# Performance work log

Measured on AMD Instinct MI355X. Metric: run time of the kernel, lower is better.

## Reference

```python
import jax, jax.numpy as jnp
import numpy as np

N_HEAD = 16
ROPE_BASE = 10000.0
RMS_EPS = 1e-6

def rms_norm(x):
    # F.rms_norm(x, (x.size(-1),)) -- no learned weight
    return x * jax.lax.rsqrt(jnp.mean(x * x, axis=-1, keepdims=True) + RMS_EPS)

def rope(x):
    # x: [B, T, H, hd]; rotate halves (non-interleaved) like the torch Rotary
    T, hd = x.shape[1], x.shape[3]
    d = hd // 2
    inv_freq = 1.0 / (ROPE_BASE ** (jnp.arange(0, hd, 2, dtype=jnp.float32) / hd))  # [d]
    t = jnp.arange(T, dtype=jnp.float32)
    freqs = jnp.outer(t, inv_freq)                       # [T, d]
    cos = jnp.cos(freqs)[None, :, None, :]
    sin = jnp.sin(freqs)[None, :, None, :]
    x1, x2 = x[..., :d], x[..., d:]
    y1 = x1 * cos + x2 * sin
    y2 = -x1 * sin + x2 * cos
    return jnp.concatenate([y1, y2], axis=-1).astype(x.dtype)

def setup_inputs() -> dict:
    key = jax.random.key(0)
    ks = jax.random.split(key, 7)
    B, T, D, H = 2, 2048, 1024, N_HEAD
    hd = D // H
    s = 0.02
    return {
        "x": jax.random.normal(ks[0], (B, T, D), jnp.float32),
        "v1": jax.random.normal(ks[1], (B, T, H, hd), jnp.float32),
        "w_q": jax.random.normal(ks[2], (D, D), jnp.float32) * s,
        "w_k": jax.random.normal(ks[3], (D, D), jnp.float32) * s,
        "w_v": jax.random.normal(ks[4], (D, D), jnp.float32) * s,
        "w_proj": jax.random.normal(ks[5], (D, D), jnp.float32) * s,
        "lamb": jnp.float32(0.5),
    }

def reference(x, v1, w_q, w_k, w_v, w_proj, lamb):
    B, T, D = x.shape
    H = N_HEAD
    hd = D // H
    q = (x @ w_q.T).reshape(B, T, H, hd)
    k = (x @ w_k.T).reshape(B, T, H, hd)
    v = (x @ w_v.T).reshape(B, T, H, hd)
    v = (1.0 - lamb) * v + lamb * v1.reshape(B, T, H, hd)
    q, k = rms_norm(q), rms_norm(k)
    q, k = rope(q), rope(k)
    scale = 1.0 / jnp.sqrt(jnp.float32(hd))
    scores = jnp.einsum('bqhd,bkhd->bhqk', q, k) * scale  # [B,H,T,T]
    causal = jnp.tril(jnp.ones((T, T), dtype=bool))
    scores = jnp.where(causal[None, None], scores, jnp.float32(-1e30))
    attn = jax.nn.softmax(scores, axis=-1)
    y = jnp.einsum('bhqk,bkhd->bqhd', attn, v).reshape(B, T, D)
    y = y @ w_proj.T
    return (y, v1)
```

## Files before the change

kernel.cpp:

```cpp
#include <hip/hip_runtime.h>

typedef __bf16 bf16x8 __attribute__((ext_vector_type(8)));
typedef float f32x4 __attribute__((ext_vector_type(4)));
typedef float f32x16 __attribute__((ext_vector_type(16)));

__device__ __forceinline__ unsigned short f2bf(float f) {
    return __builtin_bit_cast(unsigned short, (__bf16)f);
}

__device__ __forceinline__ float bf2f(unsigned short u) {
    unsigned int x = ((unsigned int)u) << 16;
    return __builtin_bit_cast(float, x);
}

__device__ __forceinline__ unsigned int packbf2(float a, float b) {
    unsigned short lo = f2bf(a), hi = f2bf(b);
    return (unsigned int)lo | ((unsigned int)hi << 16);
}

__device__ __forceinline__ bf16x8 load_frag(const unsigned short* p) {
    int4 v = *reinterpret_cast<const int4*>(p);
    return __builtin_bit_cast(bf16x8, v);
}

__device__ __forceinline__ void gload_lds16(const unsigned short* g, unsigned short* l) {
    __builtin_amdgcn_global_load_lds((const __attribute__((address_space(1))) void*)g,
                                     (__attribute__((address_space(3))) void*)l, 16, 0, 0);
}

__global__ __launch_bounds__(256) void prep_bf16(const float* __restrict__ x,
                                                 const float* __restrict__ wq,
                                                 const float* __restrict__ wk,
                                                 const float* __restrict__ wv,
                                                 const float* __restrict__ wp,
                                                 unsigned short* __restrict__ xb,
                                                 unsigned short* __restrict__ wall,
                                                 float* __restrict__ cost,
                                                 float* __restrict__ sint) {
    int bid = blockIdx.x;
    if (bid < 8192) {
        int i = (bid * 256 + threadIdx.x) * 4;
        const float* src;
        unsigned short* dst;
        int soff, doff;
        if (i < (1 << 22)) {
            src = x; dst = xb; soff = i; doff = i;
        } else {
            int j = i - (1 << 22);
            int r = j >> 20;
            src = (r == 0) ? wq : ((r == 1) ? wk : ((r == 2) ? wv : wp));
            dst = wall; soff = j & 1048575; doff = j;
        }
        float4 v = *reinterpret_cast<const float4*>(&src[soff]);
        unsigned short tmp[4] = {f2bf(v.x), f2bf(v.y), f2bf(v.z), f2bf(v.w)};
        *reinterpret_cast<int2*>(&dst[doff]) = *reinterpret_cast<int2*>(tmp);
    } else {
        int i = (bid - 8192) * 256 + threadIdx.x;
        int t = i >> 5, d = i & 31;
        float inv = powf(10000.0f, -(float)d / 32.0f);
        float f = (float)t * inv;
        cost[i] = cosf(f);
        sint[i] = sinf(f);
    }
}

__global__ __launch_bounds__(256) void gemm_bf16(const unsigned short* __restrict__ A,
                                                 const unsigned short* __restrict__ B,
                                                 unsigned short* __restrict__ C,
                                                 int N, int K) {
    __shared__ __align__(16) unsigned short As[128 * 64];
    __shared__ __align__(16) unsigned short Bs[128 * 64];
    int tid = threadIdx.x;
    int lane = tid & 63;
    int w = tid >> 6;
    int wm = w >> 1, wn = w & 1;
    int m0 = blockIdx.x * 128;
    int n0 = blockIdx.y * 128;

    f32x4 acc[4][4] = {};

    int r8 = lane >> 3;
    int csrc = (lane & 7) ^ r8;

    for (int k0 = 0; k0 < K; k0 += 64) {
        __syncthreads();
#pragma unroll
        for (int c = 0; c < 4; ++c) {
            int row = 32 * w + 8 * c + r8;
            gload_lds16(&A[(size_t)(m0 + row) * K + k0 + csrc * 8], &As[(32 * w + 8 * c) * 64]);
            gload_lds16(&B[(size_t)(n0 + row) * K + k0 + csrc * 8], &Bs[(32 * w + 8 * c) * 64]);
        }
        __syncthreads();
#pragma unroll
        for (int kk = 0; kk < 2; ++kk) {
            int col16 = kk * 4 + (lane >> 4);
            bf16x8 af[4], bfr[4];
#pragma unroll
            for (int i = 0; i < 4; ++i) {
                int row = wm * 64 + i * 16 + (lane & 15);
                af[i] = load_frag(&As[row * 64 + (col16 ^ (row & 7)) * 8]);
            }
#pragma unroll
            for (int j = 0; j < 4; ++j) {
                int row = wn * 64 + j * 16 + (lane & 15);
                bfr[j] = load_frag(&Bs[row * 64 + (col16 ^ (row & 7)) * 8]);
            }
#pragma unroll
            for (int i = 0; i < 4; ++i)
#pragma unroll
                for (int j = 0; j < 4; ++j)
                    acc[i][j] = __builtin_amdgcn_mfma_f32_16x16x32_bf16(af[i], bfr[j], acc[i][j], 0, 0, 0);
        }
    }
    int r0 = (lane >> 4) * 4;
    int cc = lane & 15;
#pragma unroll
    for (int i = 0; i < 4; ++i)
#pragma unroll
        for (int j = 0; j < 4; ++j)
#pragma unroll
            for (int r = 0; r < 4; ++r) {
                size_t m = m0 + wm * 64 + i * 16 + r0 + r;
                size_t n = n0 + wn * 64 + j * 16 + cc;
                C[m * N + n] = f2bf(acc[i][j][r]);
            }
}

__global__ __launch_bounds__(256) void gemm_proj(const unsigned short* __restrict__ pO,
                                                 const float* __restrict__ lsum,
                                                 const unsigned short* __restrict__ B,
                                                 float* __restrict__ C) {
    __shared__ __align__(16) unsigned short As[128 * 64];
    __shared__ __align__(16) unsigned short Bs[128 * 64];
    int tid = threadIdx.x;
    int lane = tid & 63;
    int w = tid >> 6;
    int wm = w >> 1, wn = w & 1;
    int m0 = blockIdx.x * 128;
    int n0 = blockIdx.y * 128;

    f32x4 acc[4][4] = {};

    int r8 = lane >> 3;
    int c8 = lane & 7;
    int csrc = c8 ^ r8;

    for (int k0 = 0; k0 < 1024; k0 += 64) {
        int h = k0 >> 6;
        __syncthreads();
#pragma unroll
        for (int c = 0; c < 4; ++c) {
            int row = 32 * w + 8 * c + r8;
            int m = m0 + row;
            int bh = ((m >> 11) << 4) + h;
            int qi = m & 2047;
            int li = bh * 2048 + qi;
            size_t pi = (size_t)li * 64 + csrc * 8;
            int4 p0 = *reinterpret_cast<const int4*>(&pO[pi]);
            int4 p1 = *reinterpret_cast<const int4*>(&pO[4194304u + pi]);
            float linv = 1.0f / (lsum[li] + lsum[65536 + li]);
            const unsigned short* u0 = reinterpret_cast<const unsigned short*>(&p0);
            const unsigned short* u1 = reinterpret_cast<const unsigned short*>(&p1);
            unsigned short tmp[8];
#pragma unroll
            for (int j = 0; j < 8; ++j) tmp[j] = f2bf((bf2f(u0[j]) + bf2f(u1[j])) * linv);
            *reinterpret_cast<int4*>(&As[row * 64 + c8 * 8]) = *reinterpret_cast<int4*>(tmp);
            gload_lds16(&B[(size_t)(n0 + row) * 1024 + k0 + csrc * 8], &Bs[(32 * w + 8 * c) * 64]);
        }
        __syncthreads();
#pragma unroll
        for (int kk = 0; kk < 2; ++kk) {
            int col16 = kk * 4 + (lane >> 4);
            bf16x8 af[4], bfr[4];
#pragma unroll
            for (int i = 0; i < 4; ++i) {
                int row = wm * 64 + i * 16 + (lane & 15);
                af[i] = load_frag(&As[row * 64 + (col16 ^ (row & 7)) * 8]);
            }
#pragma unroll
            for (int j = 0; j < 4; ++j) {
                int row = wn * 64 + j * 16 + (lane & 15);
                bfr[j] = load_frag(&Bs[row * 64 + (col16 ^ (row & 7)) * 8]);
            }
#pragma unroll
            for (int i = 0; i < 4; ++i)
#pragma unroll
                for (int j = 0; j < 4; ++j)
                    acc[i][j] = __builtin_amdgcn_mfma_f32_16x16x32_bf16(af[i], bfr[j], acc[i][j], 0, 0, 0);
        }
    }
    int r0 = (lane >> 4) * 4;
    int cc = lane & 15;
#pragma unroll
    for (int i = 0; i < 4; ++i)
#pragma unroll
        for (int j = 0; j < 4; ++j)
#pragma unroll
            for (int r = 0; r < 4; ++r) {
                size_t m = m0 + wm * 64 + i * 16 + r0 + r;
                size_t n = n0 + wn * 64 + j * 16 + cc;
                C[m * 1024 + n] = acc[i][j][r];
            }
}

__global__ __launch_bounds__(256) void post_lerp(const unsigned short* __restrict__ qkv,
                                                 const float* __restrict__ cost,
                                                 const float* __restrict__ sint,
                                                 const float* __restrict__ v1,
                                                 const float* __restrict__ lamb_p,
                                                 unsigned short* __restrict__ qb,
                                                 unsigned short* __restrict__ kb,
                                                 unsigned short* __restrict__ vt,
                                                 float* __restrict__ outv1) {
    __shared__ __align__(16) unsigned short tile[64][72];
    int bid = blockIdx.x;
    if (bid < 16384) {
        int gid = bid * 4 + (threadIdx.x >> 6);
        int lane = threadIdx.x & 63;
        int h = gid & 15;
        int t = (gid >> 4) & 2047;
        int b = gid >> 15;
        int m = b * 2048 + t;

        float q = bf2f(qkv[(size_t)m * 3072 + h * 64 + lane]);
        float k = bf2f(qkv[(size_t)m * 3072 + 1024 + h * 64 + lane]);

        float sq = q * q, sk = k * k;
        for (int msk = 1; msk < 64; msk <<= 1) {
            sq += __shfl_xor(sq, msk, 64);
            sk += __shfl_xor(sk, msk, 64);
        }
        q *= rsqrtf(sq * (1.0f / 64.0f) + 1e-6f);
        k *= rsqrtf(sk * (1.0f / 64.0f) + 1e-6f);

        int d = lane & 31;
        float c = cost[t * 32 + d], s = sint[t * 32 + d];
        float qp = __shfl_xor(q, 32, 64);
        float kp = __shfl_xor(k, 32, 64);
        float qo = (lane < 32) ? (q * c + qp * s) : (q * c - qp * s);
        float ko = (lane < 32) ? (k * c + kp * s) : (k * c - kp * s);
        qo *= 0.125f * 1.44269504088896f;

        size_t oidx = ((size_t)((b * 16 + h) * 2048 + t)) * 64 + lane;
        qb[oidx] = f2bf(qo);
        kb[oidx] = f2bf(ko);
    } else {
        int b2 = bid - 16384;
        int bh = b2 >> 5;
        int b = bh >> 4, h = bh & 15;
        int t0 = (b2 & 31) * 64;
        int tid = threadIdx.x;
        int r = tid >> 3;
        int c = (tid & 7) * 8;
        float lamb = lamb_p[0];
        float oml = 1.0f - lamb;

#pragma unroll
        for (int half = 0; half < 2; ++half) {
            int row = r + half * 32;
            int m = b * 2048 + t0 + row;
            int4 vv = *reinterpret_cast<const int4*>(&qkv[(size_t)m * 3072 + 2048 + h * 64 + c]);
            const unsigned short* vs = reinterpret_cast<const unsigned short*>(&vv);
            size_t v1i = ((size_t)m * 16 + h) * 64 + c;
            float4 va = *reinterpret_cast<const float4*>(&v1[v1i]);
            float4 vb4 = *reinterpret_cast<const float4*>(&v1[v1i + 4]);
            *reinterpret_cast<float4*>(&outv1[v1i]) = va;
            *reinterpret_cast<float4*>(&outv1[v1i + 4]) = vb4;
            float v1a[8] = {va.x, va.y, va.z, va.w, vb4.x, vb4.y, vb4.z, vb4.w};
            unsigned short tmp[8];
#pragma unroll
            for (int j = 0; j < 8; ++j) tmp[j] = f2bf(oml * bf2f(vs[j]) + lamb * v1a[j]);
            *reinterpret_cast<int4*>(&tile[row][c]) = *reinterpret_cast<int4*>(tmp);
        }
        __syncthreads();
        unsigned short* dst = vt + (size_t)bh * 64 * 2048 + t0;
        unsigned short tmp[8];
#pragma unroll
        for (int j = 0; j < 8; ++j) tmp[j] = tile[c + j][r];
        *reinterpret_cast<int4*>(&dst[(size_t)r * 2048 + c]) = *reinterpret_cast<int4*>(tmp);
#pragma unroll
        for (int j = 0; j < 8; ++j) tmp[j] = tile[c + j][r + 32];
        *reinterpret_cast<int4*>(&dst[(size_t)(r + 32) * 2048 + c]) = *reinterpret_cast<int4*>(tmp);
    }
}

__global__ __launch_bounds__(256) void attn(const unsigned short* __restrict__ qb,
                                            const unsigned short* __restrict__ kb,
                                            const unsigned short* __restrict__ vt,
                                            unsigned short* __restrict__ pO,
                                            float* __restrict__ lsum) {
    __shared__ __align__(16) unsigned short Ks[64][72];
    __shared__ __align__(16) unsigned short Vt[64][72];
    int tid = threadIdx.x;
    int lane = tid & 63;
    int w = tid >> 6;
    int hi = lane >> 5;
    int l31 = lane & 31;

    int bid = blockIdx.x;
    int bh = bid & 31;
    int r5 = bid >> 5;
    int qt = 15 - (r5 >> 1);
    int ck = r5 & 1;
    int q0 = qt * 128;
    const size_t base = (size_t)bh * 2048 * 64;
    const unsigned short* vtb = vt + (size_t)bh * 64 * 2048;
    int ktlo = ck * (qt + 1);
    int kthi = (ck + 1) * (qt + 1);

    bf16x8 qf[4];
    int qrow = q0 + w * 32 + l31;
#pragma unroll
    for (int kd = 0; kd < 4; ++kd)
        qf[kd] = load_frag(&qb[base + (size_t)qrow * 64 + kd * 16 + hi * 8]);

    f32x16 oacc[2] = {};
    float lrun = 0.0f;

    int srow = tid >> 3;
    int scol = (tid & 7) * 8;
    int4 kr0, kr1, vr0, vr1;
#define LOADT(kt_)                                                                                    \
    do {                                                                                              \
        kr0 = *reinterpret_cast<const int4*>(&kb[base + (size_t)((kt_)*64 + srow) * 64 + scol]);      \
        kr1 = *reinterpret_cast<const int4*>(&kb[base + (size_t)((kt_)*64 + srow + 32) * 64 + scol]); \
        vr0 = *reinterpret_cast<const int4*>(&vtb[(size_t)srow * 2048 + (kt_)*64 + scol]);            \
        vr1 = *reinterpret_cast<const int4*>(&vtb[(size_t)(srow + 32) * 2048 + (kt_)*64 + scol]);     \
    } while (0)

    int qwlo = q0 + w * 32;
    {
        LOADT(ktlo);
        for (int kt = ktlo; kt < kthi; ++kt) {
            __syncthreads();
            *reinterpret_cast<int4*>(&Ks[srow][scol]) = kr0;
            *reinterpret_cast<int4*>(&Ks[srow + 32][scol]) = kr1;
            *reinterpret_cast<int4*>(&Vt[srow][scol]) = vr0;
            *reinterpret_cast<int4*>(&Vt[srow + 32][scol]) = vr1;
            __syncthreads();
            if (kt + 1 < kthi) LOADT(kt + 1);

            if (kt * 64 <= qwlo + 31) {
                bool diag = (kt * 64 + 63 > qwlo);
                float rs01 = 0.0f, rs23 = 0.0f;
#pragma unroll
                for (int ntl = 0; ntl < 2; ++ntl) {
                    f32x16 sacc = {};
#pragma unroll
                    for (int kd = 0; kd < 4; ++kd) {
                        bf16x8 kf = load_frag(&Ks[ntl * 32 + l31][kd * 16 + hi * 8]);
                        sacc = __builtin_amdgcn_mfma_f32_32x32x16_bf16(kf, qf[kd], sacc, 0, 0, 0);
                    }

#pragma unroll
                    for (int r = 0; r < 16; ++r) {
                        float s = sacc[r];
                        if (diag) {
                            int kvg = kt * 64 + ntl * 32 + (r & 3) + 8 * (r >> 2) + 4 * hi;
                            if (kvg > qrow) s = -3.0e38f;
                        }
                        float e = __builtin_amdgcn_exp2f(s);
                        sacc[r] = e;
                        if (r & 2) rs23 += e; else rs01 += e;
                    }

                    unsigned int wAa[4], wBb[4];
#pragma unroll
                    for (int rr = 0; rr < 4; ++rr) {
                        wAa[rr] = packbf2(sacc[4 * rr + 0], sacc[4 * rr + 1]);
                        wBb[rr] = packbf2(sacc[4 * rr + 2], sacc[4 * rr + 3]);
                    }

#pragma unroll
                    for (int ks2 = 0; ks2 < 2; ++ks2) {
                        int b2 = ks2 * 2;
                        auto rA = __builtin_amdgcn_permlane32_swap(wAa[b2], wAa[b2 + 1], false, false);
                        auto rB = __builtin_amdgcn_permlane32_swap(wBb[b2], wBb[b2 + 1], false, false);
                        uint4 pa;
                        pa.x = rA[0];
                        pa.y = rB[0];
                        pa.z = rA[1];
                        pa.w = rB[1];
                        bf16x8 paf = __builtin_bit_cast(bf16x8, pa);
                        int ks = ntl * 2 + ks2;
#pragma unroll
                        for (int dt = 0; dt < 2; ++dt) {
                            bf16x8 vtf = load_frag(&Vt[dt * 32 + l31][ks * 16 + hi * 8]);
                            oacc[dt] = __builtin_amdgcn_mfma_f32_32x32x16_bf16(paf, vtf, oacc[dt], 0, 0, 0);
                        }
                    }
                }
                float rs = rs01 + rs23;
                rs += __shfl_xor(rs, 32, 64);
                lrun += rs;
            }
        }
    }

    unsigned short* po = pO + ((size_t)ck * 4194304u);
    float* ls = lsum + ck * 65536;
#pragma unroll
    for (int r = 0; r < 16; ++r) {
        int ql = (r & 3) + 8 * (r >> 2) + 4 * hi;
        int q = q0 + w * 32 + ql;
        size_t ro = ((size_t)bh * 2048 + q) * 64;
        po[ro + l31]      = f2bf(oacc[0][r]);
        po[ro + 32 + l31] = f2bf(oacc[1][r]);
    }
    if (hi == 0) ls[bh * 2048 + q0 + w * 32 + l31] = lrun;
#undef LOADT
}

extern "C" void kernel_launch(void* const* d_in, const int* in_sizes, int n_in,
                              void* d_out, int out_size, void* d_ws, size_t ws_size,
                              hipStream_t stream) {
    const float* x      = (const float*)d_in[0];
    const float* v1     = (const float*)d_in[1];
    const float* w_q    = (const float*)d_in[2];
    const float* w_k    = (const float*)d_in[3];
    const float* w_v    = (const float*)d_in[4];
    const float* w_proj = (const float*)d_in[5];
    const float* lamb   = (const float*)d_in[6];
    float* out = (float*)d_out;

    char* ws = (char*)d_ws;
    unsigned short* xb      = (unsigned short*)(ws + 0);
    unsigned short* wall_b  = (unsigned short*)(ws + (8u  << 20));
    unsigned short* wqkv_b  = wall_b;
    unsigned short* wproj_b = wall_b + 3u * 1048576u;
    unsigned short* qkvb    = (unsigned short*)(ws + (16u << 20));
    unsigned short* vtp     = (unsigned short*)(ws + (40u << 20));
    unsigned short* qbuf    = (unsigned short*)(ws + (48u << 20));
    unsigned short* kbuf    = (unsigned short*)(ws + (56u << 20));
    float*          cost    = (float*)        (ws + (72u << 20));
    float*          sint    = (float*)        (ws + (72u << 20) + 262144);
    unsigned short* pO      = (unsigned short*)(ws + (80u << 20));
    float*          lsum    = (float*)        (ws + (112u << 20));

    prep_bf16<<<8448, 256, 0, stream>>>(x, w_q, w_k, w_v, w_proj, xb, wall_b, cost, sint);

    gemm_bf16<<<dim3(32, 24), 256, 0, stream>>>(xb, wqkv_b, qkvb, 3072, 1024);

    post_lerp<<<17408, 256, 0, stream>>>(qkvb, cost, sint, v1, lamb, qbuf, kbuf, vtp, out + 4194304);

    attn<<<1024, 256, 0, stream>>>(qbuf, kbuf, vtp, pO, lsum);

    gemm_proj<<<dim3(32, 8), 256, 0, stream>>>(pO, lsum, wproj_b, out);
}
```

Baseline: 134.1 us.

## Fuse RMSNorm, RoPE and v-lerp into QKV GEMM epilogue

The QKV GEMM epilogue now applies RMSNorm, RoPE and the q scale directly from the accumulators and writes q/k in head-major layout. It also applies the lambda-lerp with v1 for v and writes v in head-major layout. The bf16 qkv intermediate round trip and the separate post_lerp pass go away, leaving a small transpose kernel for V. Epilogue stores are scattered 2-byte writes and the GEMM gains register pressure.

```diff
diff --git a/kernel.cpp b/kernel.cpp
--- a/kernel.cpp
+++ b/kernel.cpp
@@ -64,10 +64,16 @@
     }
 }
 
-__global__ __launch_bounds__(256) void gemm_bf16(const unsigned short* __restrict__ A,
-                                                 const unsigned short* __restrict__ B,
-                                                 unsigned short* __restrict__ C,
-                                                 int N, int K) {
+__global__ __launch_bounds__(256) void gemm_qkv(const unsigned short* __restrict__ A,
+                                                const unsigned short* __restrict__ B,
+                                                const float* __restrict__ cost,
+                                                const float* __restrict__ sint,
+                                                const float* __restrict__ v1,
+                                                const float* __restrict__ lamb_p,
+                                                unsigned short* __restrict__ qb,
+                                                unsigned short* __restrict__ kb,
+                                                unsigned short* __restrict__ vbv,
+                                                float* __restrict__ outv1) {
     __shared__ __align__(16) unsigned short As[128 * 64];
     __shared__ __align__(16) unsigned short Bs[128 * 64];
     int tid = threadIdx.x;
@@ -82,13 +88,13 @@
     int r8 = lane >> 3;
     int csrc = (lane & 7) ^ r8;
 
-    for (int k0 = 0; k0 < K; k0 += 64) {
+    for (int k0 = 0; k0 < 1024; k0 += 64) {
         __syncthreads();
 #pragma unroll
         for (int c = 0; c < 4; ++c) {
             int row = 32 * w + 8 * c + r8;
-            gload_lds16(&A[(size_t)(m0 + row) * K + k0 + csrc * 8], &As[(32 * w + 8 * c) * 64]);
-            gload_lds16(&B[(size_t)(n0 + row) * K + k0 + csrc * 8], &Bs[(32 * w + 8 * c) * 64]);
+            gload_lds16(&A[(size_t)(m0 + row) * 1024 + k0 + csrc * 8], &As[(32 * w + 8 * c) * 64]);
+            gload_lds16(&B[(size_t)(n0 + row) * 1024 + k0 + csrc * 8], &Bs[(32 * w + 8 * c) * 64]);
         }
         __syncthreads();
 #pragma unroll
@@ -112,18 +118,85 @@
                     acc[i][j] = __builtin_amdgcn_mfma_f32_16x16x32_bf16(af[i], bfr[j], acc[i][j], 0, 0, 0);
         }
     }
+
     int r0 = (lane >> 4) * 4;
     int cc = lane & 15;
-#pragma unroll
-    for (int i = 0; i < 4; ++i)
-#pragma unroll
-        for (int j = 0; j < 4; ++j)
+    int sec = blockIdx.y >> 3;
+    int hh = (blockIdx.y & 7) * 2 + wn;
+
+    if (sec < 2) {
+        unsigned short* dst = (sec == 0) ? qb : kb;
+        float sc = (sec == 0) ? (0.125f * 1.44269504088896f) : 1.0f;
+#pragma unroll
+        for (int i = 0; i < 4; ++i)
 #pragma unroll
             for (int r = 0; r < 4; ++r) {
-                size_t m = m0 + wm * 64 + i * 16 + r0 + r;
-                size_t n = n0 + wn * 64 + j * 16 + cc;
-                C[m * N + n] = f2bf(acc[i][j][r]);
-            }
+                float ss = 0.0f;
+#pragma unroll
+                for (int j = 0; j < 4; ++j) ss += acc[i][j][r] * acc[i][j][r];
+                ss += __shfl_xor(ss, 1, 64);
+                ss += __shfl_xor(ss, 2, 64);
+                ss += __shfl_xor(ss, 4, 64);
+                ss += __shfl_xor(ss, 8, 64);
+                float rn = rsqrtf(ss * (1.0f / 64.0f) + 1e-6f);
+                int mm = m0 + wm * 64 + i * 16 + r0 + r;
+                int t = mm & 2047, b = mm >> 11;
+                size_t rowb = ((size_t)((b * 16 + hh) * 2048 + t)) * 64;
+#pragma unroll
+                for (int j = 0; j < 2; ++j) {
+                    int dm = j * 16 + cc;
+                    float c = cost[t * 32 + dm], s_ = sint[t * 32 + dm];
+                    float x1 = acc[i][j][r] * rn;
+                    float x2 = acc[i][j + 2][r] * rn;
+                    dst[rowb + dm]      = f2bf((x1 * c + x2 * s_) * sc);
+                    dst[rowb + 32 + dm] = f2bf((x2 * c - x1 * s_) * sc);
+                }
+            }
+    } else {
+        float lam = lamb_p[0];
+        float oml = 1.0f - lam;
+#pragma unroll
+        for (int i = 0; i < 4; ++i)
+#pragma unroll
+            for (int r = 0; r < 4; ++r) {
+                int mm = m0 + wm * 64 + i * 16 + r0 + r;
+                int t = mm & 2047, b = mm >> 11;
+                size_t v1row = ((size_t)((b * 2048 + t) * 16 + hh)) * 64;
+                size_t vbrow = ((size_t)((b * 16 + hh) * 2048 + t)) * 64;
+#pragma unroll
+                for (int j = 0; j < 4; ++j) {
+                    int d = j * 16 + cc;
+                    float v1v = v1[v1row + d];
+                    outv1[v1row + d] = v1v;
+                    vbv[vbrow + d] = f2bf(oml * acc[i][j][r] + lam * v1v);
+                }
+            }
+    }
+}
+
+__global__ __launch_bounds__(256) void transpose_v(const unsigned short* __restrict__ vbv,
+                                                   unsigned short* __restrict__ vt) {
+    __shared__ __align__(16) unsigned short tile[64][72];
+    int bid = blockIdx.x;
+    int bh = bid >> 5;
+    int t0 = (bid & 31) * 64;
+    int tid = threadIdx.x;
+    int r = tid >> 3;
+    int c = (tid & 7) * 8;
+    const unsigned short* src = vbv + ((size_t)bh * 2048 + t0) * 64;
+    *reinterpret_cast<int4*>(&tile[r][c]) =
+        *reinterpret_cast<const int4*>(&src[(size_t)r * 64 + c]);
+    *reinterpret_cast<int4*>(&tile[r + 32][c]) =
+        *reinterpret_cast<const int4*>(&src[(size_t)(r + 32) * 64 + c]);
+    __syncthreads();
+    unsigned short* dst = vt + (size_t)bh * 64 * 2048 + t0;
+    unsigned short tmp[8];
+#pragma unroll
+    for (int j = 0; j < 8; ++j) tmp[j] = tile[c + j][r];
+    *reinterpret_cast<int4*>(&dst[(size_t)r * 2048 + c]) = *reinterpret_cast<int4*>(tmp);
+#pragma unroll
+    for (int j = 0; j < 8; ++j) tmp[j] = tile[c + j][r + 32];
+    *reinterpret_cast<int4*>(&dst[(size_t)(r + 32) * 2048 + c]) = *reinterpret_cast<int4*>(tmp);
 }
 
 __global__ __launch_bounds__(256) void gemm_proj(const unsigned short* __restrict__ pO,
@@ -203,87 +276,6 @@
             }
 }
 
-__global__ __launch_bounds__(256) void post_lerp(const unsigned short* __restrict__ qkv,
-                                                 const float* __restrict__ cost,
-                                                 const float* __restrict__ sint,
-                                                 const float* __restrict__ v1,
-                                                 const float* __restrict__ lamb_p,
-                                                 unsigned short* __restrict__ qb,
-                                                 unsigned short* __restrict__ kb,
-                                                 unsigned short* __restrict__ vt,
-                                                 float* __restrict__ outv1) {
-    __shared__ __align__(16) unsigned short tile[64][72];
-    int bid = blockIdx.x;
-    if (bid < 16384) {
-        int gid = bid * 4 + (threadIdx.x >> 6);
-        int lane = threadIdx.x & 63;
-        int h = gid & 15;
-        int t = (gid >> 4) & 2047;
-        int b = gid >> 15;
-        int m = b * 2048 + t;
-
-        float q = bf2f(qkv[(size_t)m * 3072 + h * 64 + lane]);
-        float k = bf2f(qkv[(size_t)m * 3072 + 1024 + h * 64 + lane]);
-
-        float sq = q * q, sk = k * k;
-        for (int msk = 1; msk < 64; msk <<= 1) {
-            sq += __shfl_xor(sq, msk, 64);
-            sk += __shfl_xor(sk, msk, 64);
-        }
-        q *= rsqrtf(sq * (1.0f / 64.0f) + 1e-6f);
-        k *= rsqrtf(sk * (1.0f / 64.0f) + 1e-6f);
-
-        int d = lane & 31;
-        float c = cost[t * 32 + d], s = sint[t * 32 + d];
-        float qp = __shfl_xor(q, 32, 64);
-        float kp = __shfl_xor(k, 32, 64);
-        float qo = (lane < 32) ? (q * c + qp * s) : (q * c - qp * s);
-        float ko = (lane < 32) ? (k * c + kp * s) : (k * c - kp * s);
-        qo *= 0.125f * 1.44269504088896f;
-
-        size_t oidx = ((size_t)((b * 16 + h) * 2048 + t)) * 64 + lane;
-        qb[oidx] = f2bf(qo);
-        kb[oidx] = f2bf(ko);
-    } else {
-        int b2 = bid - 16384;
-        int bh = b2 >> 5;
-        int b = bh >> 4, h = bh & 15;
-        int t0 = (b2 & 31) * 64;
-        int tid = threadIdx.x;
-        int r = tid >> 3;
-        int c = (tid & 7) * 8;
-        float lamb = lamb_p[0];
-        float oml = 1.0f - lamb;
-
-#pragma unroll
-        for (int half = 0; half < 2; ++half) {
-            int row = r + half * 32;
-            int m = b * 2048 + t0 + row;
-            int4 vv = *reinterpret_cast<const int4*>(&qkv[(size_t)m * 3072 + 2048 + h * 64 + c]);
-            const unsigned short* vs = reinterpret_cast<const unsigned short*>(&vv);
-            size_t v1i = ((size_t)m * 16 + h) * 64 + c;
-            float4 va = *reinterpret_cast<const float4*>(&v1[v1i]);
-            float4 vb4 = *reinterpret_cast<const float4*>(&v1[v1i + 4]);
-            *reinterpret_cast<float4*>(&outv1[v1i]) = va;
-            *reinterpret_cast<float4*>(&outv1[v1i + 4]) = vb4;
-            float v1a[8] = {va.x, va.y, va.z, va.w, vb4.x, vb4.y, vb4.z, vb4.w};
-            unsigned short tmp[8];
-#pragma unroll
-            for (int j = 0; j < 8; ++j) tmp[j] = f2bf(oml * bf2f(vs[j]) + lamb * v1a[j]);
-            *reinterpret_cast<int4*>(&tile[row][c]) = *reinterpret_cast<int4*>(tmp);
-        }
-        __syncthreads();
-        unsigned short* dst = vt + (size_t)bh * 64 * 2048 + t0;
-        unsigned short tmp[8];
-#pragma unroll
-        for (int j = 0; j < 8; ++j) tmp[j] = tile[c + j][r];
-        *reinterpret_cast<int4*>(&dst[(size_t)r * 2048 + c]) = *reinterpret_cast<int4*>(tmp);
-#pragma unroll
-        for (int j = 0; j < 8; ++j) tmp[j] = tile[c + j][r + 32];
-        *reinterpret_cast<int4*>(&dst[(size_t)(r + 32) * 2048 + c]) = *reinterpret_cast<int4*>(tmp);
-    }
-}
-
 __global__ __launch_bounds__(256) void attn(const unsigned short* __restrict__ qb,
                                             const unsigned short* __restrict__ kb,
                                             const unsigned short* __restrict__ vt,
@@ -428,7 +420,7 @@
     unsigned short* wall_b  = (unsigned short*)(ws + (8u  << 20));
     unsigned short* wqkv_b  = wall_b;
     unsigned short* wproj_b = wall_b + 3u * 1048576u;
-    unsigned short* qkvb    = (unsigned short*)(ws + (16u << 20));
+    unsigned short* vbuf    = (unsigned short*)(ws + (16u << 20));
     unsigned short* vtp     = (unsigned short*)(ws + (40u << 20));
     unsigned short* qbuf    = (unsigned short*)(ws + (48u << 20));
     unsigned short* kbuf    = (unsigned short*)(ws + (56u << 20));
@@ -439,9 +431,10 @@
 
     prep_bf16<<<8448, 256, 0, stream>>>(x, w_q, w_k, w_v, w_proj, xb, wall_b, cost, sint);
 
-    gemm_bf16<<<dim3(32, 24), 256, 0, stream>>>(xb, wqkv_b, qkvb, 3072, 1024);
-
-    post_lerp<<<17408, 256, 0, stream>>>(qkvb, cost, sint, v1, lamb, qbuf, kbuf, vtp, out + 4194304);
+    gemm_qkv<<<dim3(32, 24), 256, 0, stream>>>(xb, wqkv_b, cost, sint, v1, lamb,
+                                               qbuf, kbuf, vbuf, out + 4194304);
+
+    transpose_v<<<1024, 256, 0, stream>>>(vbuf, vtp);
 
     attn<<<1024, 256, 0, stream>>>(qbuf, kbuf, vtp, pO, lsum);
 
```

Result: faster. 130.5 us (-2.6%).
